# Performance work log

Hardware: AMD Instinct MI355X
Metric: run time of the kernel (lower is better)

## Reference

```python
import jax, jax.numpy as jnp
import numpy as np

DIM = 64   # model dim == d_inner (expand=1)
Hh = 64
Ww = 64
BATCH = 4
D_IN = 64
N_ST = 8   # d_state
DT_R = 4   # dt_rank = ceil(dim/16)
K = 4      # depthwise conv kernel
NB = 8     # total CrossMambaBlocks: 4 (depth=1) + 4 final cross blocks


def setup_inputs():
    key = jax.random.key(0)
    ks = iter(jax.random.split(key, 40))
    def rn(shape, s=0.02):
        return jax.random.normal(next(ks), shape, jnp.float32) * s
    A_init = jnp.log(jnp.tile(jnp.arange(1, N_ST + 1, dtype=jnp.float32), (NB, D_IN, 1)))
    return dict(
        img1=rn((BATCH, DIM, Hh, Ww), 1.0), img2=rn((BATCH, DIM, Hh, Ww), 1.0),
        img1_sum=rn((BATCH, DIM, Hh, Ww), 1.0), img2_sum=rn((BATCH, DIM, Hh, Ww), 1.0),
        norm0_w=jnp.ones((NB, DIM)), norm0_b=jnp.zeros((NB, DIM)),
        norm1_w=jnp.ones((NB, DIM)), norm1_b=jnp.zeros((NB, DIM)),
        in_w=rn((NB, 2 * D_IN, DIM)), in_b=jnp.zeros((NB, 2 * D_IN)),
        conv_w_f=rn((NB, D_IN, 1, K), 0.1), conv_b_f=jnp.zeros((NB, D_IN)),
        conv_w_b=rn((NB, D_IN, 1, K), 0.1), conv_b_b=jnp.zeros((NB, D_IN)),
        xproj_w_f=rn((NB, DT_R + 2 * N_ST, D_IN)), xproj_w_b=rn((NB, DT_R + 2 * N_ST, D_IN)),
        dtproj_w_f=rn((NB, D_IN, DT_R), 0.1), dtproj_b_f=jnp.zeros((NB, D_IN)),
        dtproj_w_b=rn((NB, D_IN, DT_R), 0.1), dtproj_b_b=jnp.zeros((NB, D_IN)),
        A_log_f=A_init, A_log_b=A_init,
        D_f=jnp.ones((NB, D_IN)), D_b=jnp.ones((NB, D_IN)),
        ln_w=jnp.ones((NB, D_IN)), ln_b=jnp.zeros((NB, D_IN)),
        mout_w=rn((NB, DIM, D_IN)), mout_b=jnp.zeros((NB, DIM)),
        fop_w=rn((DIM, 2 * DIM)), fop_b=jnp.zeros((DIM,)),
    )


def _ln(x, w, b):
    m = x.mean(-1, keepdims=True)
    v = ((x - m) ** 2).mean(-1, keepdims=True)
    return (x - m) * jax.lax.rsqrt(v + 1e-5) * w + b


def _dwconv(x, w, b):
    # x: [b,L,d], w: [d,1,K] depthwise causal conv along L
    y = jax.lax.conv_general_dilated(
        x.transpose(0, 2, 1), w, (1,), [(K - 1, 0)],
        dimension_numbers=('NCH', 'OIH', 'NCH'),
        feature_group_count=x.shape[-1])
    return y.transpose(0, 2, 1) + b


def _ssm(u, dt, Bm, Cm, A, Dm):
    # u,dt: [b,L,d]; Bm,Cm: [b,L,n]; A: [d,n]; Dm: [d]
    dA = jnp.exp(dt[..., None] * A)                 # [b,L,d,n]
    dBu = (dt * u)[..., None] * Bm[:, :, None, :]   # [b,L,d,n]
    def step(h, xs):
        dA_t, dBu_t, C_t = xs
        h = dA_t * h + dBu_t
        return h, jnp.einsum('bdn,bn->bd', h, C_t)
    h0 = jnp.zeros(u.shape[:1] + A.shape, u.dtype)
    _, ys = jax.lax.scan(step, h0, (jnp.moveaxis(dA, 1, 0), jnp.moveaxis(dBu, 1, 0), jnp.moveaxis(Cm, 1, 0)))
    return jnp.moveaxis(ys, 0, 1) + u * Dm


def _direction(x_in, extra, conv_w, conv_b, xproj_w, dtproj_w, dtproj_b, A_log, Dm, flip):
    if flip:
        x_in = x_in[:, ::-1]
        extra = extra[:, ::-1]
    u = jax.nn.silu(_dwconv(x_in, conv_w, conv_b))
    dbl = jnp.einsum('bld,ed->ble', extra, xproj_w)     # cross: dt/B/C from extra embedding
    dtr = dbl[..., :DT_R]
    Bm = dbl[..., DT_R:DT_R + N_ST]
    Cm = dbl[..., DT_R + N_ST:]
    dt = jax.nn.softplus(jnp.einsum('blr,dr->bld', dtr, dtproj_w) + dtproj_b)
    y = _ssm(u, dt, Bm, Cm, -jnp.exp(A_log), Dm)
    if flip:
        y = y[:, ::-1]
    return y


def _cross_block(i, x, extra, p):
    skip = x
    x = _ln(x, p['norm0_w'][i], p['norm0_b'][i])
    extra = _ln(extra, p['norm1_w'][i], p['norm1_b'][i])
    xz = jnp.einsum('bld,ed->ble', x, p['in_w'][i]) + p['in_b'][i]
    x_in, z = xz[..., :D_IN], xz[..., D_IN:]
    y_f = _direction(x_in, extra, p['conv_w_f'][i], p['conv_b_f'][i], p['xproj_w_f'][i],
                     p['dtproj_w_f'][i], p['dtproj_b_f'][i], p['A_log_f'][i], p['D_f'][i], False)
    y_b = _direction(x_in, extra, p['conv_w_b'][i], p['conv_b_b'][i], p['xproj_w_b'][i],
                     p['dtproj_w_b'][i], p['dtproj_b_b'][i], p['A_log_b'][i], p['D_b'][i], True)
    y = 0.5 * (y_f + y_b)                    # if_devide_out=True
    y = _ln(y, p['ln_w'][i], p['ln_b'][i])   # use_norm=True
    y = y * jax.nn.silu(z)
    out = jnp.einsum('bld,ed->ble', y, p['mout_w'][i]) + p['mout_b'][i]
    return out + skip


def _forward(img1, img2, img1_sum, img2_sum, norm0_w, norm0_b, norm1_w, norm1_b, in_w, in_b,
             conv_w_f, conv_b_f, conv_w_b, conv_b_b, xproj_w_f, xproj_w_b,
             dtproj_w_f, dtproj_b_f, dtproj_w_b, dtproj_b_b, A_log_f, A_log_b,
             D_f, D_b, ln_w, ln_b, mout_w, mout_b, fop_w, fop_b):
    p = dict(norm0_w=norm0_w, norm0_b=norm0_b, norm1_w=norm1_w, norm1_b=norm1_b,
             in_w=in_w, in_b=in_b, conv_w_f=conv_w_f, conv_b_f=conv_b_f,
             conv_w_b=conv_w_b, conv_b_b=conv_b_b, xproj_w_f=xproj_w_f, xproj_w_b=xproj_w_b,
             dtproj_w_f=dtproj_w_f, dtproj_b_f=dtproj_b_f, dtproj_w_b=dtproj_w_b,
             dtproj_b_b=dtproj_b_b, A_log_f=A_log_f, A_log_b=A_log_b, D_f=D_f, D_b=D_b,
             ln_w=ln_w, ln_b=ln_b, mout_w=mout_w, mout_b=mout_b)
    def seq(t):
        b, c, h, w = t.shape
        return t.reshape(b, c, h * w).transpose(0, 2, 1)   # b (h w) c
    s1, s2, s1s, s2s = seq(img1), seq(img2), seq(img1_sum), seq(img2_sum)
    # depth=1 cross-fusion loop
    s1 = _cross_block(0, s1, s1s, p)
    s2 = _cross_block(1, s2, s2s, p)
    s1s = _cross_block(2, s1s, s1, p)
    s2s = _cross_block(3, s2s, s2, p)
    # final cross blocks
    i1l = _cross_block(4, s1, s2, p)
    i1g = _cross_block(5, s1, s2s, p)
    i2l = _cross_block(6, s2, s1, p)
    i2g = _cross_block(7, s2, s1s, p)
    c1 = jnp.concatenate([i1l, i1g], -1)
    c2 = jnp.concatenate([i2l, i2g], -1)
    fusion = jnp.einsum('ble,ce->blc', 0.5 * (c1 + c2), fop_w) + fop_b
    b = img1.shape[0]
    return fusion.transpose(0, 2, 1).reshape(b, DIM, Hh, Ww)


def reference(img1, img2, img1_sum, img2_sum, norm0_w, norm0_b, norm1_w, norm1_b, in_w, in_b,
              conv_w_f, conv_b_f, conv_w_b, conv_b_b, xproj_w_f, xproj_w_b,
              dtproj_w_f, dtproj_b_f, dtproj_w_b, dtproj_b_b, A_log_f, A_log_b,
              D_f, D_b, ln_w, ln_b, mout_w, mout_b, fop_w, fop_b):
    return _forward(img1, img2, img1_sum, img2_sum, norm0_w, norm0_b, norm1_w, norm1_b, in_w, in_b,
                    conv_w_f, conv_b_f, conv_w_b, conv_b_b, xproj_w_f, xproj_w_b,
                    dtproj_w_f, dtproj_b_f, dtproj_w_b, dtproj_b_b, A_log_f, A_log_b,
                    D_f, D_b, ln_w, ln_b, mout_w, mout_b, fop_w, fop_b)
```

## Files before the change

kernel.cpp:

```cpp
#include <hip/hip_runtime.h>
#include <hip/hip_bf16.h>

#define BX 4
#define LX 4096
#define DX 64
#define NX 8
#define TCH 16
#define NCH 256
#define BLD (BX*LX*DX)

typedef unsigned short u16;
typedef __attribute__((ext_vector_type(8))) short v8s;
typedef __attribute__((ext_vector_type(4))) float v4f;

#define L2E 1.44269504088896f
#define LN2 0.69314718055994531f

__device__ __forceinline__ float b2f(u16 u){ return __uint_as_float(((unsigned)u)<<16); }
__device__ __forceinline__ u16 f2b(float f){
  unsigned u = __float_as_uint(f);
  unsigned r = (u + 0x7FFFu + ((u>>16)&1u)) >> 16;
  return (u16)r;
}
__device__ __forceinline__ float siluf(float x){
  return x * __builtin_amdgcn_rcpf(1.f + __builtin_amdgcn_exp2f(-x*L2E));
}
__device__ __forceinline__ float softplusf(float x){
  const float t = __builtin_amdgcn_exp2f(-fabsf(x)*L2E);
  return fmaxf(x, 0.f) + LN2 * __builtin_amdgcn_logf(1.f + t);
}

__device__ __forceinline__ v4f mfma16(v8s a, v8s b, v4f c){
  return __builtin_amdgcn_mfma_f32_16x16x32_bf16(a, b, c, 0, 0, 0);
}
__device__ __forceinline__ void split8(const float* v, v8s& hi, v8s& lo){
  #pragma unroll
  for(int j=0;j<8;j++){
    const short h = (short)f2b(v[j]);
    hi[j] = h;
    lo[j] = (short)f2b(v[j] - b2f((u16)h));
  }
}
__device__ __forceinline__ void afrag(const float* tile, int lane, int k0, v8s& hi, v8s& lo){
  const float* p = tile + (lane&15)*72 + k0 + ((lane>>4)<<3);
  float v[8];
  const float4 a = *(const float4*)(p);
  const float4 b = *(const float4*)(p+4);
  v[0]=a.x; v[1]=a.y; v[2]=a.z; v[3]=a.w;
  v[4]=b.x; v[5]=b.y; v[6]=b.z; v[7]=b.w;
  split8(v, hi, lo);
}

struct Ctx {
  const float *nw0,*nb0,*nw1,*nb1;
  const float *inb;
  const float *convw,*convb;
  const float *dtw,*dtb;
  const float *A2,*Dp;
  const float *lnw,*lnb;
  const float *moutb;
  const float *fopb;
  const u16 *wih,*wil,*wxh,*wxl,*wmh,*wml,*wfh,*wfl;
  float *act[4], *outc[4];
  float *xin[4], *zz[4], *dbl[4], *yy[4], *Pp[4], *qq[4], *hin[4];
};

struct BlkDesc { int i; const float* x; const float* e; float* out; int slot; };
struct StageArgs { BlkDesc d[4]; };

struct PrepEnt { const void* src; float* dst; int n; int mode; };
struct PrepAll { PrepEnt a[21]; };
struct WPrep { const void* sA; const void* sB; u16* dh; u16* dl; long off; int E; int KS; int kind; int i; };
struct WPrepAll { WPrep a[25]; };

__global__ __launch_bounds__(256) void k_prep(PrepAll pa, WPrepAll wa, const u16* df){
  const bool isbf = (df[0] == 0x3F80u);
  if(blockIdx.y < 21){
    PrepEnt p = pa.a[blockIdx.y];
    int idx = blockIdx.x*256 + threadIdx.x;
    if(idx < p.n){
      float v = isbf ? b2f(((const u16*)p.src)[idx]) : ((const float*)p.src)[idx];
      if(p.mode==2) v = -__expf(v) * L2E;
      p.dst[idx] = v;
    }
  } else {
    WPrep p = wa.a[blockIdx.y - 21];
    const int wv = threadIdx.x >> 6, lane = threadIdx.x & 63;
    const int idx = blockIdx.x*4 + wv;
    const int NT = (p.E + 15) >> 4;
    if(idx >= NT*p.KS) return;
    const int ct = idx / p.KS, ks = idx % p.KS;
    const int g  = ct*16 + (lane & 15);
    const int k0 = ks*32 + ((lane>>4)<<3);
    const int K  = p.KS*32;
    bool valid; long si = 0; const void* sp = p.sA;
    if(p.kind == 1){
      valid = (g < 40);
      const int dir = g/20, e = g - dir*20;
      if(dir) sp = p.sB;
      si = ((long)p.i*20 + e)*64 + k0;
    } else {
      valid = (g < p.E);
      si = p.off + (long)g*K + k0;
    }
    float v[8];
    #pragma unroll
    for(int j2=0;j2<8;j2++){
      float x = 0.f;
      if(valid) x = isbf ? b2f(((const u16*)sp)[si+j2]) : ((const float*)sp)[si+j2];
      v[j2] = x;
    }
    v8s hi, lo; split8(v, hi, lo);
    const size_t o = ((size_t)idx*64 + lane)*8;
    *(v8s*)(p.dh + o) = hi;
    *(v8s*)(p.dl + o) = lo;
  }
}

struct SeqArgs { const void* src[4]; };

__global__ __launch_bounds__(256) void k_seq(SeqArgs s, Ctx c, const u16* df){
  const bool isbf = (df[0] == 0x3F80u);
  __shared__ float ld[64*65];
  const int t = blockIdx.z, b = blockIdx.y, l0 = blockIdx.x*64;
  float* dst = c.act[t];
  const int tx = threadIdx.x, ty = threadIdx.y;
  if(isbf){
    const u16* src = (const u16*)s.src[t];
    #pragma unroll
    for(int k=0;k<16;k++){ int d = k*4+ty; ld[d*65+tx] = b2f(src[(size_t)(b*64+d)*LX + l0+tx]); }
  } else {
    const float* src = (const float*)s.src[t];
    #pragma unroll
    for(int k=0;k<16;k++){ int d = k*4+ty; ld[d*65+tx] = src[(size_t)(b*64+d)*LX + l0+tx]; }
  }
  __syncthreads();
  #pragma unroll
  for(int k=0;k<16;k++){ int p = k*4+ty; dst[(size_t)(b*LX + l0+p)*64 + tx] = ld[tx*65+p]; }
}

__device__ __forceinline__ void coop72(float* sb, const float* g, int t){
  #pragma unroll
  for(int k=0;k<4;k++){
    const int idx = k*256 + t;
    const int row = idx >> 4;
    const int c4  = (idx & 15) << 2;
    *(float4*)(sb + row*72 + c4) = *(const float4*)(g + (size_t)row*64 + c4);
  }
}
__device__ __forceinline__ void coop72_avg(float* sb, const float* g0, const float* g1, int t){
  #pragma unroll
  for(int k=0;k<4;k++){
    const int idx = k*256 + t;
    const int row = idx >> 4;
    const int c4  = (idx & 15) << 2;
    const float4 a = *(const float4*)(g0 + (size_t)row*64 + c4);
    const float4 b = *(const float4*)(g1 + (size_t)row*64 + c4);
    float4 o; o.x=0.5f*(a.x+b.x); o.y=0.5f*(a.y+b.y); o.z=0.5f*(a.z+b.z); o.w=0.5f*(a.w+b.w);
    *(float4*)(sb + row*72 + c4) = o;
  }
}

__device__ __forceinline__ void ln72(float* sb, int lane, const float* w, const float* b){
  float r[64];
  float* p = sb + lane*72;
  #pragma unroll
  for(int cc=0;cc<64;cc+=4){ float4 v = *(const float4*)(p+cc); r[cc]=v.x; r[cc+1]=v.y; r[cc+2]=v.z; r[cc+3]=v.w; }
  float m=0.f;
  #pragma unroll
  for(int d=0;d<64;d++) m += r[d];
  m *= (1.f/64.f);
  float va=0.f;
  #pragma unroll
  for(int d=0;d<64;d++){ float t=r[d]-m; va += t*t; }
  va *= (1.f/64.f);
  const float rs = rsqrtf(va + 1e-5f);
  #pragma unroll
  for(int d=0;d<64;d++) r[d] = (r[d]-m)*rs*w[d] + b[d];
  #pragma unroll
  for(int cc=0;cc<64;cc+=4){ float4 v={r[cc],r[cc+1],r[cc+2],r[cc+3]}; *(float4*)(p+cc)=v; }
}

__global__ __launch_bounds__(256) void k_front(Ctx c, StageArgs sa){
  __shared__ __align__(16) float sx[64*72];
  __shared__ __align__(16) float se[64*72];
  const BlkDesc bd = sa.d[blockIdx.y];
  const int i = bd.i;
  const int tile = blockIdx.x;
  const int b = tile >> 6;
  const int l0 = (tile & 63) << 6;
  const int bl0 = b*LX + l0;
  const int t = threadIdx.x;
  const int wave = t >> 6, lane = t & 63;

  coop72(sx, bd.x + (size_t)bl0*64, t);
  coop72(se, bd.e + (size_t)bl0*64, t);
  __syncthreads();
  if(wave == 0)      ln72(sx, lane, c.nw0 + i*64, c.nb0 + i*64);
  else if(wave == 1) ln72(se, lane, c.nw1 + i*64, c.nb1 + i*64);
  __syncthreads();

  const int m0 = wave*16;
  const int q  = lane >> 4;
  const int n15 = lane & 15;

  {
    v8s ah[2], al[2];
    afrag(sx + m0*72, lane, 0,  ah[0], al[0]);
    afrag(sx + m0*72, lane, 32, ah[1], al[1]);
    const v8s* WH = (const v8s*)c.wih + (size_t)i*1024;
    const v8s* WL = (const v8s*)c.wil + (size_t)i*1024;
    #pragma unroll 1
    for(int ct=0; ct<8; ct++){
      const int colg = ct*16 + n15;
      const float bias = c.inb[i*128 + colg];
      v4f acc = {bias, bias, bias, bias};
      #pragma unroll
      for(int ks=0; ks<2; ks++){
        const v8s wh = WH[(ct*2+ks)*64 + lane];
        const v8s wl = WL[(ct*2+ks)*64 + lane];
        acc = mfma16(ah[ks], wl, acc);
        acc = mfma16(al[ks], wh, acc);
        acc = mfma16(ah[ks], wh, acc);
      }
      float* baseo = (colg < 64) ? c.xin[bd.slot] : c.zz[bd.slot];
      const int col = colg & 63;
      #pragma unroll
      for(int r=0;r<4;r++){
        const int row = m0 + q*4 + r;
        baseo[(size_t)(bl0+row)*64 + col] = acc[r];
      }
    }
  }
  {
    v8s ah[2], al[2];
    afrag(se + m0*72, lane, 0,  ah[0], al[0]);
    afrag(se + m0*72, lane, 32, ah[1], al[1]);
    const v8s* WH = (const v8s*)c.wxh + (size_t)i*384;
    const v8s* WL = (const v8s*)c.wxl + (size_t)i*384;
    #pragma unroll 1
    for(int ct=0; ct<3; ct++){
      v4f acc = {0.f,0.f,0.f,0.f};
      #pragma unroll
      for(int ks=0; ks<2; ks++){
        const v8s wh = WH[(ct*2+ks)*64 + lane];
        const v8s wl = WL[(ct*2+ks)*64 + lane];
        acc = mfma16(ah[ks], wl, acc);
        acc = mfma16(al[ks], wh, acc);
        acc = mfma16(ah[ks], wh, acc);
      }
      const int g = ct*16 + n15;
      if(g < 40){
        const int dir = (g >= 20);
        const int e = g - dir*20;
        float* dp = c.dbl[bd.slot] + (size_t)dir*((size_t)BX*LX*20);
        #pragma unroll
        for(int r=0;r<4;r++){
          const int row = m0 + q*4 + r;
          dp[(size_t)(bl0+row)*20 + e] = acc[r];
        }
      }
    }
  }
}

template<int PASS>
__device__ __forceinline__ void scan_body(const Ctx& c, const StageArgs& sa){
  __shared__ __align__(16) float meta[TCH*20];
  const int zid = blockIdx.z;
  const int j = zid >> 1, dir = zid & 1;
  const BlkDesc bd = sa.d[j];
  const int i = bd.i, slot = bd.slot;
  const int ch = blockIdx.x, b = blockIdx.y;
  const int d = threadIdx.x;
  const int pb = (dir*8 + i)*64 + d;

  const float4 cwv = *(const float4*)(c.convw + (size_t)pb*4);
  const float  cbv = c.convb[pb];
  const float4 dwv = *(const float4*)(c.dtw + (size_t)pb*4);
  const float  dtbv = c.dtb[pb];
  const float4 A2a = *(const float4*)(c.A2 + (size_t)pb*8);
  const float4 A2b = *(const float4*)(c.A2 + (size_t)pb*8 + 4);
  float A2[8] = {A2a.x,A2a.y,A2a.z,A2a.w,A2b.x,A2b.y,A2b.z,A2b.w};

  {
    const float4* s = (const float4*)(c.dbl[slot] + (size_t)dir*((size_t)BX*LX*20)
                                      + (size_t)(b*LX + ch*TCH)*20);
    float4* dst = (float4*)meta;
    #pragma unroll
    for(int k=0;k<2;k++){ int idx = k*64 + d; if(idx < 80) dst[idx] = s[idx]; }
  }
  __syncthreads();

  const float* X = c.xin[slot] + (size_t)b*LX*64 + d;
  float h[8];
  if(PASS==1){
    #pragma unroll
    for(int n=0;n<8;n++) h[n]=0.f;
  } else {
    const float* hp = c.hin[slot] + (size_t)(dir*NCH + ch)*((size_t)BX*512) + (size_t)b*512 + d;
    #pragma unroll
    for(int n=0;n<8;n++) h[n] = hp[n*64];
  }
  const float Dv = (PASS==3) ? c.Dp[pb] : 0.f;
  float* Y = (PASS==3) ? (c.yy[slot] + (size_t)(dir*BX + b)*LX*64 + d) : (float*)0;

  int lbase, sgn;
  if(dir==0){ lbase = ch*TCH;          sgn =  1; }
  else      { lbase = ch*TCH + TCH-1;  sgn = -1; }
  float w0,w1,w2;
  { int p0 = lbase - 3*sgn; w0 = (p0>=0 && p0<LX)? X[(size_t)p0*64] : 0.f; }
  { int p1 = lbase - 2*sgn; w1 = (p1>=0 && p1<LX)? X[(size_t)p1*64] : 0.f; }
  { int p2 = lbase - 1*sgn; w2 = (p2>=0 && p2<LX)? X[(size_t)p2*64] : 0.f; }

  const float* Xp = X + (size_t)lbase*64;
  float* Yp = (PASS==3) ? (Y + (size_t)lbase*64) : (float*)0;
  const float* mp = meta + (dir ? (TCH-1)*20 : 0);
  const int xstep = sgn*64;
  const int mstep = sgn*20;

  float S = 0.f;
  #pragma unroll 4
  for(int t=0;t<TCH;t++){
    const float xc = *Xp;
    const float u = siluf(cwv.x*w0 + cwv.y*w1 + cwv.z*w2 + cwv.w*xc + cbv);
    const float4 m0  = *(const float4*)(mp);
    const float4 mb0 = *(const float4*)(mp+4);
    const float4 mb1 = *(const float4*)(mp+8);
    const float dt = softplusf(m0.x*dwv.x + m0.y*dwv.y + m0.z*dwv.z + m0.w*dwv.w + dtbv);
    const float du = dt*u;
    const float Bv[8] = {mb0.x,mb0.y,mb0.z,mb0.w,mb1.x,mb1.y,mb1.z,mb1.w};
    #pragma unroll
    for(int n=0;n<8;n++){
      const float dA = __builtin_amdgcn_exp2f(dt*A2[n]);
      h[n] = dA*h[n] + du*Bv[n];
    }
    if(PASS==3){
      const float4 mc0 = *(const float4*)(mp+12);
      const float4 mc1 = *(const float4*)(mp+16);
      const float Cv[8] = {mc0.x,mc0.y,mc0.z,mc0.w,mc1.x,mc1.y,mc1.z,mc1.w};
      float yv = u*Dv;
      #pragma unroll
      for(int n=0;n<8;n++) yv += h[n]*Cv[n];
      *Yp = yv;
      Yp += xstep;
    } else {
      S += dt;
    }
    w0=w1; w1=w2; w2=xc;
    Xp += xstep; mp += mstep;
  }
  if(PASS==1){
    float* Pw = c.Pp[slot] + (size_t)(dir*NCH + ch)*((size_t)BX*512) + (size_t)b*512 + d;
    float* Qw = c.qq[slot] + (size_t)(dir*NCH + ch)*((size_t)BX*512) + (size_t)b*512 + d;
    #pragma unroll
    for(int n=0;n<8;n++){
      Pw[n*64] = __builtin_amdgcn_exp2f(A2[n]*S);
      Qw[n*64] = h[n];
    }
  }
}

__global__ __launch_bounds__(64) void k_scan1(Ctx c, StageArgs sa){ scan_body<1>(c, sa); }
__global__ __launch_bounds__(64) void k_scan3(Ctx c, StageArgs sa){ scan_body<3>(c, sa); }

__global__ __launch_bounds__(64) void k_mid(Ctx c, StageArgs sa){
  const int b = blockIdx.x >> 3;
  const int seg = blockIdx.x & 7;
  const int dir = blockIdx.y & 1, j = blockIdx.y >> 1;
  const BlkDesc bd = sa.d[j];
  const int slot = bd.slot;
  const int nd = seg*64 + threadIdx.x;
  const size_t base = (size_t)dir*NCH*((size_t)BX*512) + (size_t)b*512 + nd;
  const size_t STR = (size_t)BX*512;
  const float* P = c.Pp[slot] + base;
  const float* Q = c.qq[slot] + base;
  float* H = c.hin[slot] + base;
  float h = 0.f;
  float Pv[32], Qv[32];
  #pragma unroll 1
  for(int g=0; g<NCH/32; g++){
    #pragma unroll
    for(int k=0;k<32;k++){
      const int ch = dir ? (NCH-1 - (g*32+k)) : (g*32+k);
      Pv[k] = P[(size_t)ch*STR]; Qv[k] = Q[(size_t)ch*STR];
    }
    #pragma unroll
    for(int k=0;k<32;k++){
      const int ch = dir ? (NCH-1 - (g*32+k)) : (g*32+k);
      H[(size_t)ch*STR] = h;
      h = fmaf(Pv[k], h, Qv[k]);
    }
  }
}

__global__ __launch_bounds__(256) void k_back(Ctx c, StageArgs sa){
  __shared__ __align__(16) float sy[64*72];
  __shared__ __align__(16) float sz[64*72];
  __shared__ __align__(16) float sk[64*72];
  const BlkDesc bd = sa.d[blockIdx.y];
  const int i = bd.i, slot = bd.slot;
  const int tile = blockIdx.x;
  const int b = tile >> 6;
  const int l0 = (tile & 63) << 6;
  const int bl0 = b*LX + l0;
  const int t = threadIdx.x;
  const int wave = t >> 6, lane = t & 63;

  coop72_avg(sy, c.yy[slot] + (size_t)b*LX*64 + (size_t)l0*64,
                 c.yy[slot] + (size_t)(BX+b)*LX*64 + (size_t)l0*64, t);
  coop72(sz, c.zz[slot] + (size_t)bl0*64, t);
  coop72(sk, bd.x + (size_t)bl0*64, t);
  __syncthreads();
  if(wave == 0){
    ln72(sy, lane, c.lnw + i*64, c.lnb + i*64);
    float* p = sy + lane*72;
    const float* zp = sz + lane*72;
    #pragma unroll
    for(int d=0;d<64;d++){ p[d] *= siluf(zp[d]); }
  }
  __syncthreads();

  const int m0 = wave*16;
  const int q  = lane >> 4;
  const int n15 = lane & 15;
  v8s ah[2], al[2];
  afrag(sy + m0*72, lane, 0,  ah[0], al[0]);
  afrag(sy + m0*72, lane, 32, ah[1], al[1]);
  const v8s* WH = (const v8s*)c.wmh + (size_t)i*512;
  const v8s* WL = (const v8s*)c.wml + (size_t)i*512;
  #pragma unroll 1
  for(int ct=0; ct<4; ct++){
    const int col = ct*16 + n15;
    const float bias = c.moutb[i*64 + col];
    v4f acc = {bias, bias, bias, bias};
    #pragma unroll
    for(int ks=0; ks<2; ks++){
      const v8s wh = WH[(ct*2+ks)*64 + lane];
      const v8s wl = WL[(ct*2+ks)*64 + lane];
      acc = mfma16(ah[ks], wl, acc);
      acc = mfma16(al[ks], wh, acc);
      acc = mfma16(ah[ks], wh, acc);
    }
    #pragma unroll
    for(int r=0;r<4;r++){
      const int row = m0 + q*4 + r;
      bd.out[(size_t)(bl0+row)*64 + col] = acc[r] + sk[row*72 + col];
    }
  }
}

__global__ __launch_bounds__(256) void k_fusion(Ctx c, void* outp, const u16* df){
  const bool isbf = (df[0] == 0x3F80u);
  __shared__ __align__(16) float sL[64*72];
  __shared__ __align__(16) float sH[64*72];
  __shared__ __align__(16) float sT[64*68];
  const int tile = blockIdx.x;
  const int b = tile >> 6;
  const int l0 = (tile & 63) << 6;
  const int bl0 = b*LX + l0;
  const int t = threadIdx.x;
  const int wave = t >> 6, lane = t & 63;

  coop72_avg(sL, c.outc[0] + (size_t)bl0*64, c.outc[2] + (size_t)bl0*64, t);
  coop72_avg(sH, c.outc[1] + (size_t)bl0*64, c.outc[3] + (size_t)bl0*64, t);
  __syncthreads();

  const int m0 = wave*16;
  const int q  = lane >> 4;
  const int n15 = lane & 15;
  v8s ah[4], al[4];
  afrag(sL + m0*72, lane, 0,  ah[0], al[0]);
  afrag(sL + m0*72, lane, 32, ah[1], al[1]);
  afrag(sH + m0*72, lane, 0,  ah[2], al[2]);
  afrag(sH + m0*72, lane, 32, ah[3], al[3]);
  const v8s* WH = (const v8s*)c.wfh;
  const v8s* WL = (const v8s*)c.wfl;
  #pragma unroll 1
  for(int ct=0; ct<4; ct++){
    const int col = ct*16 + n15;
    const float bias = c.fopb[col];
    v4f acc = {bias, bias, bias, bias};
    #pragma unroll
    for(int ks=0; ks<4; ks++){
      const v8s wh = WH[(ct*4+ks)*64 + lane];
      const v8s wl = WL[(ct*4+ks)*64 + lane];
      acc = mfma16(ah[ks], wl, acc);
      acc = mfma16(al[ks], wh, acc);
      acc = mfma16(ah[ks], wh, acc);
    }
    #pragma unroll
    for(int r=0;r<4;r++) sT[col*68 + m0 + q*4 + r] = acc[r];
  }
  __syncthreads();

  const int o  = t >> 2;
  const int p0 = (t & 3) * 16;
  float v[16];
  #pragma unroll
  for(int k=0;k<16;k+=4){
    const float4 x = *(const float4*)(sT + o*68 + p0 + k);
    v[k]=x.x; v[k+1]=x.y; v[k+2]=x.z; v[k+3]=x.w;
  }
  const size_t off = (size_t)(b*64+o)*LX + l0 + p0;
  if(isbf){
    u16 hb[16];
    #pragma unroll
    for(int k=0;k<16;k++) hb[k] = f2b(v[k]);
    uint4 u0, u1;
    u0.x = hb[0] | ((unsigned)hb[1]<<16);  u0.y = hb[2] | ((unsigned)hb[3]<<16);
    u0.z = hb[4] | ((unsigned)hb[5]<<16);  u0.w = hb[6] | ((unsigned)hb[7]<<16);
    u1.x = hb[8] | ((unsigned)hb[9]<<16);  u1.y = hb[10]| ((unsigned)hb[11]<<16);
    u1.z = hb[12]| ((unsigned)hb[13]<<16); u1.w = hb[14]| ((unsigned)hb[15]<<16);
    *(uint4*)((u16*)outp + off)     = u0;
    *(uint4*)((u16*)outp + off + 8) = u1;
  } else {
    float* fo = (float*)outp + off;
    #pragma unroll
    for(int k=0;k<16;k+=4){ float4 x={v[k],v[k+1],v[k+2],v[k+3]}; *(float4*)(fo+k)=x; }
  }
}

extern "C" void kernel_launch(void* const* d_in, const int* in_sizes, int n_in,
                              void* d_out, int out_size, void* d_ws, size_t ws_size,
                              hipStream_t stream){
  (void)in_sizes; (void)out_size;
  if(n_in < 30) return;
  const u16* df = (const u16*)d_in[22];
  float* w = (float*)d_ws;
  size_t off = 0;
  auto al = [&](size_t n){ float* p = w + off; off += n; return p; };

  Ctx c;
  float* nw0 = al(512);  float* nb0 = al(512);
  float* nw1 = al(512);  float* nb1 = al(512);
  float* inb = al(1024);
  float* convw = al(4096); float* convb = al(1024);
  float* dtw = al(4096); float* dtb = al(1024);
  float* A2 = al(8192);  float* Dp = al(1024);
  float* lnw = al(512);  float* lnb = al(512);
  float* moutb = al(512);
  float* fopb = al(64);
  c.nw0=nw0; c.nb0=nb0; c.nw1=nw1; c.nb1=nb1;
  c.inb=inb; c.convw=convw; c.convb=convb;
  c.dtw=dtw; c.dtb=dtb; c.A2=A2; c.Dp=Dp;
  c.lnw=lnw; c.lnb=lnb; c.moutb=moutb; c.fopb=fopb;

  u16* wih = (u16*)al(32768); u16* wil = (u16*)al(32768);
  u16* wxh = (u16*)al(12288); u16* wxl = (u16*)al(12288);
  u16* wmh = (u16*)al(16384); u16* wml = (u16*)al(16384);
  u16* wfh = (u16*)al(4096);  u16* wfl = (u16*)al(4096);
  c.wih=wih; c.wil=wil; c.wxh=wxh; c.wxl=wxl; c.wmh=wmh; c.wml=wml; c.wfh=wfh; c.wfl=wfl;

  for(int k=0;k<4;k++) c.act[k]  = al(BLD);
  for(int k=0;k<4;k++) c.outc[k] = al(BLD);

  const size_t CHW = 2*(size_t)NCH*BX*512;
  const size_t SLOT = (size_t)BLD + BLD + 2*(size_t)BX*LX*20 + 2*(size_t)BLD + 3*CHW;
  const size_t avail = ws_size/4;
  int nslots = 4;
  while(nslots>1 && off + (size_t)nslots*SLOT > avail) nslots >>= 1;
  for(int s=0;s<nslots;s++){
    c.xin[s]=al(BLD); c.zz[s]=al(BLD); c.dbl[s]=al(2*(size_t)BX*LX*20);
    c.yy[s]=al(2*(size_t)BLD);
    c.Pp[s]=al(CHW); c.qq[s]=al(CHW); c.hin[s]=al(CHW);
  }
  for(int s=nslots;s<4;s++){
    c.xin[s]=c.xin[0]; c.zz[s]=c.zz[0]; c.dbl[s]=c.dbl[0]; c.yy[s]=c.yy[0];
    c.Pp[s]=c.Pp[0]; c.qq[s]=c.qq[0]; c.hin[s]=c.hin[0];
  }

  PrepAll pa;
  int kk = 0;
  auto add = [&](int idx, float* dst, int n, int mode){
    pa.a[kk].src=d_in[idx]; pa.a[kk].dst=dst; pa.a[kk].n=n; pa.a[kk].mode=mode; kk++;
  };
  add(4,  nw0, 512, 0); add(5,  nb0, 512, 0);
  add(6,  nw1, 512, 0); add(7,  nb1, 512, 0);
  add(9,  inb, 1024, 0);
  add(10, convw, 2048, 0);      add(11, convb, 512, 0);
  add(12, convw+2048, 2048, 0); add(13, convb+512, 512, 0);
  add(16, dtw, 2048, 0);        add(17, dtb, 512, 0);
  add(18, dtw+2048, 2048, 0);   add(19, dtb+512, 512, 0);
  add(20, A2, 4096, 2);         add(21, A2+4096, 4096, 2);
  add(22, Dp, 512, 0);          add(23, Dp+512, 512, 0);
  add(24, lnw, 512, 0);         add(25, lnb, 512, 0);
  add(27, moutb, 512, 0);
  add(29, fopb, 64, 0);

  WPrepAll wa;
  for(int i=0;i<8;i++) wa.a[i]    = { d_in[8],  nullptr,  wih+(size_t)i*8192, wil+(size_t)i*8192, (long)i*8192, 128, 2, 0, i };
  for(int i=0;i<8;i++) wa.a[8+i]  = { d_in[14], d_in[15], wxh+(size_t)i*3072, wxl+(size_t)i*3072, 0,            48, 2, 1, i };
  for(int i=0;i<8;i++) wa.a[16+i] = { d_in[26], nullptr,  wmh+(size_t)i*4096, wml+(size_t)i*4096, (long)i*4096, 64, 2, 0, i };
  wa.a[24] = { d_in[28], nullptr, wfh, wfl, 0, 64, 4, 0, 0 };

  k_prep<<<dim3(16,46),256,0,stream>>>(pa, wa, df);

  SeqArgs sq;
  for(int t=0;t<4;t++) sq.src[t] = d_in[t];
  k_seq<<<dim3(64,BX,4), dim3(64,4), 0, stream>>>(sq, c, df);

  BlkDesc R1[2] = {{0, c.act[0], c.act[2], c.act[0], 0},
                   {1, c.act[1], c.act[3], c.act[1], 0}};
  BlkDesc R2[4] = {{2, c.act[2], c.act[0], c.act[2], 0},
                   {3, c.act[3], c.act[1], c.act[3], 0},
                   {4, c.act[0], c.act[1], c.outc[0], 0},
                   {6, c.act[1], c.act[0], c.outc[2], 0}};
  BlkDesc R3[2] = {{5, c.act[0], c.act[3], c.outc[1], 0},
                   {7, c.act[1], c.act[2], c.outc[3], 0}};

  auto run = [&](BlkDesc* ds, int cnt){
    for(int k=0;k<cnt;k+=nslots){
      int n = cnt-k; if(n>nslots) n = nslots;
      StageArgs sa;
      for(int j=0;j<n;j++){ sa.d[j] = ds[k+j]; sa.d[j].slot = j; }
      for(int j=n;j<4;j++) sa.d[j] = sa.d[0];
      k_front<<<dim3(256,n),      256, 0, stream>>>(c, sa);
      k_scan1<<<dim3(NCH,BX,2*n),  64, 0, stream>>>(c, sa);
      k_mid  <<<dim3(BX*8,2*n),    64, 0, stream>>>(c, sa);
      k_scan3<<<dim3(NCH,BX,2*n),  64, 0, stream>>>(c, sa);
      k_back <<<dim3(256,n),      256, 0, stream>>>(c, sa);
    }
  };
  run(R1,2); run(R2,4); run(R3,2);
  k_fusion<<<256,256,0,stream>>>(c, d_out, df);
}
```

Measured before the change: 376.5 us.

## Fuse second scan pass into back-projection kernel and drop yy buffer

Removes the separate k_scan3 launch by recomputing the chunk-local scan with output y inside k_back. Each wave covers one 16-step chunk for both directions and accumulates the averaged y directly into shared memory, so the yy global buffer and its round trip go away. k_scan1 now preloads its conv window into registers and is specialised per direction with full unrolling. z and the residual are read straight from global memory instead of being staged in LDS. The cost is more register pressure and serial scan work inside k_back, which has only 4 waves per block.

```diff
diff --git a/kernel.cpp b/kernel.cpp
--- a/kernel.cpp
+++ b/kernel.cpp
@@ -62,7 +62,7 @@
   const float *fopb;
   const u16 *wih,*wil,*wxh,*wxl,*wmh,*wml,*wfh,*wfl;
   float *act[4], *outc[4];
-  float *xin[4], *zz[4], *dbl[4], *yy[4], *Pp[4], *qq[4], *hin[4];
+  float *xin[4], *zz[4], *dbl[4], *Pp[4], *qq[4], *hin[4];
 };
 
 struct BlkDesc { int i; const float* x; const float* e; float* out; int slot; };
@@ -264,8 +264,33 @@
   }
 }
 
-template<int PASS>
-__device__ __forceinline__ void scan_body(const Ctx& c, const StageArgs& sa){
+template<int DIR>
+__device__ __forceinline__ void scan1_dir(const float* xs, const float* meta,
+    const float4 cwv, const float cbv, const float4 dwv, const float dtbv,
+    const float* A2, float* h, float& S){
+  #pragma unroll
+  for(int t=0;t<TCH;t++){
+    float w0,w1,w2,xc; int lr;
+    if(DIR==0){ lr=t;       w0=xs[t];    w1=xs[t+1];  w2=xs[t+2];  xc=xs[t+3]; }
+    else      { lr=15-t;    w0=xs[18-t]; w1=xs[17-t]; w2=xs[16-t]; xc=xs[15-t]; }
+    const float u = siluf(cwv.x*w0 + cwv.y*w1 + cwv.z*w2 + cwv.w*xc + cbv);
+    const float* m = meta + lr*20;
+    const float4 m0 = *(const float4*)(m);
+    const float dt = softplusf(m0.x*dwv.x + m0.y*dwv.y + m0.z*dwv.z + m0.w*dwv.w + dtbv);
+    const float du = dt*u;
+    const float4 mb0 = *(const float4*)(m+4);
+    const float4 mb1 = *(const float4*)(m+8);
+    const float Bv[8] = {mb0.x,mb0.y,mb0.z,mb0.w,mb1.x,mb1.y,mb1.z,mb1.w};
+    #pragma unroll
+    for(int n=0;n<8;n++){
+      const float dA = __builtin_amdgcn_exp2f(dt*A2[n]);
+      h[n] = dA*h[n] + du*Bv[n];
+    }
+    S += dt;
+  }
+}
+
+__global__ __launch_bounds__(64) void k_scan1(Ctx c, StageArgs sa){
   __shared__ __align__(16) float meta[TCH*20];
   const int zid = blockIdx.z;
   const int j = zid >> 1, dir = zid & 1;
@@ -292,77 +317,32 @@
   }
   __syncthreads();
 
+  const int base = ch*TCH;
   const float* X = c.xin[slot] + (size_t)b*LX*64 + d;
+  float xs[19];
+  if(dir==0){
+    #pragma unroll
+    for(int k=0;k<19;k++){ const int r = base - 3 + k; xs[k] = (r>=0) ? X[(size_t)r*64] : 0.f; }
+  } else {
+    #pragma unroll
+    for(int k=0;k<19;k++){ const int r = base + k; xs[k] = (r<LX) ? X[(size_t)r*64] : 0.f; }
+  }
+
   float h[8];
-  if(PASS==1){
-    #pragma unroll
-    for(int n=0;n<8;n++) h[n]=0.f;
-  } else {
-    const float* hp = c.hin[slot] + (size_t)(dir*NCH + ch)*((size_t)BX*512) + (size_t)b*512 + d;
-    #pragma unroll
-    for(int n=0;n<8;n++) h[n] = hp[n*64];
-  }
-  const float Dv = (PASS==3) ? c.Dp[pb] : 0.f;
-  float* Y = (PASS==3) ? (c.yy[slot] + (size_t)(dir*BX + b)*LX*64 + d) : (float*)0;
-
-  int lbase, sgn;
-  if(dir==0){ lbase = ch*TCH;          sgn =  1; }
-  else      { lbase = ch*TCH + TCH-1;  sgn = -1; }
-  float w0,w1,w2;
-  { int p0 = lbase - 3*sgn; w0 = (p0>=0 && p0<LX)? X[(size_t)p0*64] : 0.f; }
-  { int p1 = lbase - 2*sgn; w1 = (p1>=0 && p1<LX)? X[(size_t)p1*64] : 0.f; }
-  { int p2 = lbase - 1*sgn; w2 = (p2>=0 && p2<LX)? X[(size_t)p2*64] : 0.f; }
-
-  const float* Xp = X + (size_t)lbase*64;
-  float* Yp = (PASS==3) ? (Y + (size_t)lbase*64) : (float*)0;
-  const float* mp = meta + (dir ? (TCH-1)*20 : 0);
-  const int xstep = sgn*64;
-  const int mstep = sgn*20;
-
+  #pragma unroll
+  for(int n=0;n<8;n++) h[n]=0.f;
   float S = 0.f;
-  #pragma unroll 4
-  for(int t=0;t<TCH;t++){
-    const float xc = *Xp;
-    const float u = siluf(cwv.x*w0 + cwv.y*w1 + cwv.z*w2 + cwv.w*xc + cbv);
-    const float4 m0  = *(const float4*)(mp);
-    const float4 mb0 = *(const float4*)(mp+4);
-    const float4 mb1 = *(const float4*)(mp+8);
-    const float dt = softplusf(m0.x*dwv.x + m0.y*dwv.y + m0.z*dwv.z + m0.w*dwv.w + dtbv);
-    const float du = dt*u;
-    const float Bv[8] = {mb0.x,mb0.y,mb0.z,mb0.w,mb1.x,mb1.y,mb1.z,mb1.w};
-    #pragma unroll
-    for(int n=0;n<8;n++){
-      const float dA = __builtin_amdgcn_exp2f(dt*A2[n]);
-      h[n] = dA*h[n] + du*Bv[n];
-    }
-    if(PASS==3){
-      const float4 mc0 = *(const float4*)(mp+12);
-      const float4 mc1 = *(const float4*)(mp+16);
-      const float Cv[8] = {mc0.x,mc0.y,mc0.z,mc0.w,mc1.x,mc1.y,mc1.z,mc1.w};
-      float yv = u*Dv;
-      #pragma unroll
-      for(int n=0;n<8;n++) yv += h[n]*Cv[n];
-      *Yp = yv;
-      Yp += xstep;
-    } else {
-      S += dt;
-    }
-    w0=w1; w1=w2; w2=xc;
-    Xp += xstep; mp += mstep;
-  }
-  if(PASS==1){
-    float* Pw = c.Pp[slot] + (size_t)(dir*NCH + ch)*((size_t)BX*512) + (size_t)b*512 + d;
-    float* Qw = c.qq[slot] + (size_t)(dir*NCH + ch)*((size_t)BX*512) + (size_t)b*512 + d;
-    #pragma unroll
-    for(int n=0;n<8;n++){
-      Pw[n*64] = __builtin_amdgcn_exp2f(A2[n]*S);
-      Qw[n*64] = h[n];
-    }
-  }
-}
-
-__global__ __launch_bounds__(64) void k_scan1(Ctx c, StageArgs sa){ scan_body<1>(c, sa); }
-__global__ __launch_bounds__(64) void k_scan3(Ctx c, StageArgs sa){ scan_body<3>(c, sa); }
+  if(dir==0) scan1_dir<0>(xs, meta, cwv, cbv, dwv, dtbv, A2, h, S);
+  else       scan1_dir<1>(xs, meta, cwv, cbv, dwv, dtbv, A2, h, S);
+
+  float* Pw = c.Pp[slot] + (size_t)(dir*NCH + ch)*((size_t)BX*512) + (size_t)b*512 + d;
+  float* Qw = c.qq[slot] + (size_t)(dir*NCH + ch)*((size_t)BX*512) + (size_t)b*512 + d;
+  #pragma unroll
+  for(int n=0;n<8;n++){
+    Pw[n*64] = __builtin_amdgcn_exp2f(A2[n]*S);
+    Qw[n*64] = h[n];
+  }
+}
 
 __global__ __launch_bounds__(64) void k_mid(Ctx c, StageArgs sa){
   const int b = blockIdx.x >> 3;
@@ -396,8 +376,7 @@
 
 __global__ __launch_bounds__(256) void k_back(Ctx c, StageArgs sa){
   __shared__ __align__(16) float sy[64*72];
-  __shared__ __align__(16) float sz[64*72];
-  __shared__ __align__(16) float sk[64*72];
+  __shared__ __align__(16) float smeta[64*40];
   const BlkDesc bd = sa.d[blockIdx.y];
   const int i = bd.i, slot = bd.slot;
   const int tile = blockIdx.x;
@@ -407,21 +386,87 @@
   const int t = threadIdx.x;
   const int wave = t >> 6, lane = t & 63;
 
-  coop72_avg(sy, c.yy[slot] + (size_t)b*LX*64 + (size_t)l0*64,
-                 c.yy[slot] + (size_t)(BX+b)*LX*64 + (size_t)l0*64, t);
-  coop72(sz, c.zz[slot] + (size_t)bl0*64, t);
-  coop72(sk, bd.x + (size_t)bl0*64, t);
+  #pragma unroll
+  for(int d2=0; d2<2; d2++){
+    const float4* s = (const float4*)(c.dbl[slot] + (size_t)d2*((size_t)BX*LX*20) + (size_t)bl0*20);
+    #pragma unroll
+    for(int k=0;k<2;k++){
+      const int idx = k*256 + t;
+      if(idx < 320){
+        const int row = idx/5, e4 = idx - row*5;
+        *(float4*)(smeta + row*40 + d2*20 + e4*4) = s[idx];
+      }
+    }
+  }
+  __syncthreads();
+
+  const int m0 = wave*16;
+  {
+    const int ch = (tile & 63)*4 + wave;
+    const int d2 = lane;
+    const float* X = c.xin[slot] + (size_t)b*LX*64 + d2;
+    float xs[22];
+    #pragma unroll
+    for(int k=0;k<22;k++){
+      const int r = l0 + m0 + k - 3;
+      xs[k] = (r>=0 && r<LX) ? X[(size_t)r*64] : 0.f;
+    }
+    #pragma unroll
+    for(int dir=0; dir<2; dir++){
+      const int pb = (dir*8 + i)*64 + d2;
+      const float4 cwv = *(const float4*)(c.convw + (size_t)pb*4);
+      const float  cbv = c.convb[pb];
+      const float4 dwv = *(const float4*)(c.dtw + (size_t)pb*4);
+      const float  dtbv = c.dtb[pb];
+      const float4 A2a = *(const float4*)(c.A2 + (size_t)pb*8);
+      const float4 A2b = *(const float4*)(c.A2 + (size_t)pb*8 + 4);
+      const float A2r[8] = {A2a.x,A2a.y,A2a.z,A2a.w,A2b.x,A2b.y,A2b.z,A2b.w};
+      const float Dv = c.Dp[pb];
+      float h[8];
+      const float* hp = c.hin[slot] + (size_t)(dir*NCH + ch)*((size_t)BX*512) + (size_t)b*512 + d2;
+      #pragma unroll
+      for(int n=0;n<8;n++) h[n] = hp[n*64];
+      #pragma unroll
+      for(int k=0;k<16;k++){
+        const int lr = dir ? (m0+15-k) : (m0+k);
+        const float w0 = dir ? xs[21-k] : xs[k];
+        const float w1 = dir ? xs[20-k] : xs[k+1];
+        const float w2 = dir ? xs[19-k] : xs[k+2];
+        const float xc = dir ? xs[18-k] : xs[k+3];
+        const float u = siluf(cwv.x*w0 + cwv.y*w1 + cwv.z*w2 + cwv.w*xc + cbv);
+        const float* m = smeta + lr*40 + dir*20;
+        const float4 m0v = *(const float4*)(m);
+        const float dt = softplusf(m0v.x*dwv.x + m0v.y*dwv.y + m0v.z*dwv.z + m0v.w*dwv.w + dtbv);
+        const float du = dt*u;
+        const float4 mb0 = *(const float4*)(m+4);
+        const float4 mb1 = *(const float4*)(m+8);
+        const float Bv[8] = {mb0.x,mb0.y,mb0.z,mb0.w,mb1.x,mb1.y,mb1.z,mb1.w};
+        float yv = u*Dv;
+        #pragma unroll
+        for(int n=0;n<8;n++){
+          const float dA = __builtin_amdgcn_exp2f(dt*A2r[n]);
+          h[n] = dA*h[n] + du*Bv[n];
+        }
+        const float4 mc0 = *(const float4*)(m+12);
+        const float4 mc1 = *(const float4*)(m+16);
+        const float Cv[8] = {mc0.x,mc0.y,mc0.z,mc0.w,mc1.x,mc1.y,mc1.z,mc1.w};
+        #pragma unroll
+        for(int n=0;n<8;n++) yv += h[n]*Cv[n];
+        if(dir==0) sy[lr*72 + d2] = 0.5f*yv;
+        else       sy[lr*72 + d2] += 0.5f*yv;
+      }
+    }
+  }
   __syncthreads();
   if(wave == 0){
     ln72(sy, lane, c.lnw + i*64, c.lnb + i*64);
     float* p = sy + lane*72;
-    const float* zp = sz + lane*72;
-    #pragma unroll
-    for(int d=0;d<64;d++){ p[d] *= siluf(zp[d]); }
-  }
-  __syncthreads();
-
-  const int m0 = wave*16;
+    const float* zp = c.zz[slot] + (size_t)(bl0+lane)*64;
+    #pragma unroll
+    for(int d3=0;d3<64;d3++){ p[d3] *= siluf(zp[d3]); }
+  }
+  __syncthreads();
+
   const int q  = lane >> 4;
   const int n15 = lane & 15;
   v8s ah[2], al[2];
@@ -445,7 +490,7 @@
     #pragma unroll
     for(int r=0;r<4;r++){
       const int row = m0 + q*4 + r;
-      bd.out[(size_t)(bl0+row)*64 + col] = acc[r] + sk[row*72 + col];
+      bd.out[(size_t)(bl0+row)*64 + col] = acc[r] + bd.x[(size_t)(bl0+row)*64 + col];
     }
   }
 }
@@ -556,17 +601,16 @@
   for(int k=0;k<4;k++) c.outc[k] = al(BLD);
 
   const size_t CHW = 2*(size_t)NCH*BX*512;
-  const size_t SLOT = (size_t)BLD + BLD + 2*(size_t)BX*LX*20 + 2*(size_t)BLD + 3*CHW;
+  const size_t SLOT = (size_t)BLD + BLD + 2*(size_t)BX*LX*20 + 3*CHW;
   const size_t avail = ws_size/4;
   int nslots = 4;
   while(nslots>1 && off + (size_t)nslots*SLOT > avail) nslots >>= 1;
   for(int s=0;s<nslots;s++){
     c.xin[s]=al(BLD); c.zz[s]=al(BLD); c.dbl[s]=al(2*(size_t)BX*LX*20);
-    c.yy[s]=al(2*(size_t)BLD);
     c.Pp[s]=al(CHW); c.qq[s]=al(CHW); c.hin[s]=al(CHW);
   }
   for(int s=nslots;s<4;s++){
-    c.xin[s]=c.xin[0]; c.zz[s]=c.zz[0]; c.dbl[s]=c.dbl[0]; c.yy[s]=c.yy[0];
+    c.xin[s]=c.xin[0]; c.zz[s]=c.zz[0]; c.dbl[s]=c.dbl[0];
     c.Pp[s]=c.Pp[0]; c.qq[s]=c.qq[0]; c.hin[s]=c.hin[0];
   }
 
@@ -618,7 +662,6 @@
       k_front<<<dim3(256,n),      256, 0, stream>>>(c, sa);
       k_scan1<<<dim3(NCH,BX,2*n),  64, 0, stream>>>(c, sa);
       k_mid  <<<dim3(BX*8,2*n),    64, 0, stream>>>(c, sa);
-      k_scan3<<<dim3(NCH,BX,2*n),  64, 0, stream>>>(c, sa);
       k_back <<<dim3(256,n),      256, 0, stream>>>(c, sa);
     }
   };
```

Result: faster. 352.7 us (-6.3%).
